# Kernel optimization log

Hardware: AMD Instinct MI355X
Metric: run time of the kernel (lower is better)

## Reference

```python
import jax, jax.numpy as jnp
import numpy as np
import itertools

BND = 64            # spatial_shape[0]; coords clamped to [0, BND] inclusive
G = BND + 1         # voxel grid side
OFFSETS = np.array(list(itertools.product([-1, 0, 1], repeat=3)), dtype=np.int32)  # [27,3], k=3, pad=1


def setup_inputs() -> dict:
    key = jax.random.key(0)
    k1, k2, k3 = jax.random.split(key, 3)
    B, H, W, C = 16, 64, 64, 256
    depth = jax.random.uniform(k1, (B, H, W), dtype=jnp.float32)
    N = B * (H * W + 1)  # +1 cls coord per batch row
    features = jax.random.normal(k2, (N, C), dtype=jnp.float32)
    # SubMConv3d weight, one [C_in, C_out] matrix per kernel offset (27 taps).
    # (Original zero-inits this weight; random values used for a meaningful baseline.)
    weight = jax.random.normal(k3, (27, C, C), dtype=jnp.float32) * 0.02
    return {"features": features, "depth": depth, "weight": weight}


def _coords(depth):
    # generate_3d_coords_from_depth + quantization from forward()
    B, H, W = depth.shape
    y, x = jnp.meshgrid(jnp.arange(H, dtype=jnp.float32) / (H - 1),
                        jnp.arange(W, dtype=jnp.float32) / (W - 1), indexing='ij')
    zmin = depth.min(axis=(1, 2), keepdims=True)
    zmax = depth.max(axis=(1, 2), keepdims=True)
    z = (depth - zmin) / (zmax - zmin + 1e-8)
    coords = jnp.stack([jnp.broadcast_to(x, (B, H, W)),
                        jnp.broadcast_to(y, (B, H, W)), z], axis=-1)  # [B,H,W,3]
    coord = coords.reshape(B, H * W, 3)
    coord = jnp.clip(jnp.round(coord * BND), 0, BND).astype(jnp.int32)
    cls = jnp.zeros((B, 1, 3), dtype=jnp.int32)  # cls token coord per batch row
    return jnp.concatenate([cls, coord], axis=1).reshape(-1, 3)  # [N,3]


def _subm_conv(features, coord, weight):
    # Submanifold sparse 3D conv: output only at active sites; gather active
    # neighbors per kernel offset, GEMM, accumulate.
    N = features.shape[0]
    lin = (coord[:, 0] * G + coord[:, 1]) * G + coord[:, 2]  # [N]
    # voxel -> point-index map; duplicates resolved deterministically via max
    idx_map = jnp.full((G * G * G,), -1, dtype=jnp.int32).at[lin].max(
        jnp.arange(N, dtype=jnp.int32))
    offs = jnp.asarray(OFFSETS)                      # [27,3]
    nb = coord[None, :, :] + offs[:, None, :]        # [27,N,3]
    inb = jnp.all((nb >= 0) & (nb <= BND), axis=-1)  # [27,N]
    nbc = jnp.clip(nb, 0, BND)
    nlin = (nbc[..., 0] * G + nbc[..., 1]) * G + nbc[..., 2]
    nid = idx_map[nlin]                              # [27,N]
    valid = inb & (nid >= 0)

    def body(acc, xs):
        nid_k, val_k, Wk = xs
        g = jnp.where(val_k[:, None], features[jnp.maximum(nid_k, 0)], 0.0)  # gather [N,C]
        return acc + g @ Wk, None

    out0 = jnp.zeros((N, weight.shape[-1]), dtype=features.dtype)
    out, _ = jax.lax.scan(body, out0, (nid, valid, weight))  # 27 gather-GEMM steps
    return out


def reference(features, depth, weight):
    coord = _coords(depth)
    return _subm_conv(features.astype(jnp.float32), coord, weight)
```

## Files before the change

### kernel.cpp

```cpp
#include <hip/hip_runtime.h>

#define NPTS 65552
#define MPAD 65664
#define NVOX 274625

typedef unsigned short u16;
typedef __attribute__((ext_vector_type(8))) short bf16x8;
typedef __attribute__((ext_vector_type(4))) float f32x4;
typedef __attribute__((ext_vector_type(4))) unsigned short us4;

__device__ __forceinline__ u16 f2bf(float f) {
  unsigned int u = __float_as_uint(f);
  return (u16)((u + 0x7FFFu + ((u >> 16) & 1u)) >> 16);
}

__global__ void coords_kernel(const float* __restrict__ depth, int* __restrict__ pcoord) {
  int b = blockIdx.x, tid = threadIdx.x;
  const float* d = depth + b * 4096;
  float mn = 1e30f, mx = -1e30f;
  for (int p = tid; p < 4096; p += 256) {
    float v = d[p];
    mn = fminf(mn, v);
    mx = fmaxf(mx, v);
  }
  __shared__ float smn[256], smx[256];
  smn[tid] = mn; smx[tid] = mx;
  __syncthreads();
  for (int s = 128; s > 0; s >>= 1) {
    if (tid < s) {
      smn[tid] = fminf(smn[tid], smn[tid + s]);
      smx[tid] = fmaxf(smx[tid], smx[tid + s]);
    }
    __syncthreads();
  }
  mn = smn[0]; mx = smx[0];
  float den = mx - mn + 1e-8f;
  for (int p = tid; p < 4096; p += 256) {
    int i = p >> 6, j = p & 63;
    float x = (float)j / 63.0f;
    float y = (float)i / 63.0f;
    float z = (d[p] - mn) / den;
    int cx = (int)rintf(x * 64.0f);
    int cy = (int)rintf(y * 64.0f);
    int cz = (int)rintf(z * 64.0f);
    cx = min(max(cx, 0), 64); cy = min(max(cy, 0), 64); cz = min(max(cz, 0), 64);
    pcoord[b * 4097 + 1 + p] = cx | (cy << 8) | (cz << 16);
  }
  if (tid == 0) pcoord[b * 4097] = 0;
}

__global__ void init_idx(int* __restrict__ m) {
  int i = blockIdx.x * 256 + threadIdx.x;
  if (i < NVOX) m[i] = -1;
}

__global__ void scatter_idx(const int* __restrict__ pcoord, int* __restrict__ m) {
  int n = blockIdx.x * 256 + threadIdx.x;
  if (n >= NPTS) return;
  int c = pcoord[n];
  int lin = ((c & 255) * 65 + ((c >> 8) & 255)) * 65 + ((c >> 16) & 255);
  atomicMax(&m[lin], n);
}

__global__ void nbr_kernel(const int* __restrict__ pcoord, const int* __restrict__ m,
                           int* __restrict__ nid) {
  int n = blockIdx.x * 256 + threadIdx.x;
  if (n >= MPAD) return;
  if (n >= NPTS) {
    for (int k = 0; k < 27; ++k) nid[k * MPAD + n] = NPTS;
    return;
  }
  int c = pcoord[n];
  int cx = c & 255, cy = (c >> 8) & 255, cz = (c >> 16) & 255;
#pragma unroll
  for (int k = 0; k < 27; ++k) {
    int nx = cx + k / 9 - 1;
    int ny = cy + (k / 3) % 3 - 1;
    int nz = cz + k % 3 - 1;
    int id = NPTS;
    if (((unsigned)nx <= 64u) && ((unsigned)ny <= 64u) && ((unsigned)nz <= 64u)) {
      int v = m[(nx * 65 + ny) * 65 + nz];
      if (v >= 0) id = v;
    }
    nid[k * MPAD + n] = id;
  }
}

__global__ void conv_feat(const float* __restrict__ f, u16* __restrict__ o) {
  int q = blockIdx.x * 256 + threadIdx.x;
  if (q >= (NPTS + 1) * 64) return;
  us4 r;
  if (q < NPTS * 64) {
    float4 v = ((const float4*)f)[q];
    r.x = f2bf(v.x); r.y = f2bf(v.y); r.z = f2bf(v.z); r.w = f2bf(v.w);
  } else {
    r.x = 0; r.y = 0; r.z = 0; r.w = 0;
  }
  ((us4*)o)[q] = r;
}

__global__ void conv_wt2(const float* __restrict__ w, u16* __restrict__ wt2) {
  int u = blockIdx.x * 256 + threadIdx.x;
  int e = u & 7, row = (u >> 3) & 255, lk = (u >> 11) & 3, ks = (u >> 13) & 7, ko = u >> 16;
  int ci = ks * 32 + lk * 8 + e;
  wt2[u] = f2bf(w[ko * 65536 + ci * 256 + row]);
}

__device__ __forceinline__ void gload16(const void* g, unsigned int lds_off) {
  __builtin_amdgcn_global_load_lds(
      (__attribute__((address_space(1))) void*)(size_t)g,
      (__attribute__((address_space(3))) void*)(unsigned int)lds_off,
      16, 0, 0);
}

__global__ __launch_bounds__(512) void gemm_kernel(const u16* __restrict__ feat,
                                                   const u16* __restrict__ wt,
                                                   const int* __restrict__ nid,
                                                   float* __restrict__ out) {
  __shared__ u16 As[3 * 4096];
  __shared__ u16 Bs[3 * 8192];
  int bm = blockIdx.x;
  int tid = threadIdx.x;
  int w = tid >> 6, l = tid & 63;
  int wr = w >> 2, wc = w & 3;
  int lm = l & 15, lk = l >> 4;

  unsigned A0 = (unsigned)(size_t)&As[0];
  unsigned B0 = (unsigned)(size_t)&Bs[0];
  const char* Asc = (const char*)&As[0];
  const char* Bsc = (const char*)&Bs[0];

  const char* featc = (const char*)feat;
  const char* wtc = (const char*)wt;

  int row_l = (w << 4) + (l >> 2);
  int gmA = bm * 128 + row_l;
  int cA16 = (((l & 3) ^ ((row_l >> 1) & 3)) << 4);
  int aswz = lk ^ ((lm >> 1) & 3);

  f32x4 acc[4][4];
#pragma unroll
  for (int m = 0; m < 4; ++m)
#pragma unroll
    for (int n = 0; n < 4; ++n) acc[m][n] = (f32x4){0.f, 0.f, 0.f, 0.f};

  int nv = nid[gmA];
  int nv_next = nv;

  {
    gload16(featc + ((size_t)nv << 9) + cA16, A0 + (w << 10));
    const char* bs0 = wtc + (w << 11) + (l << 4);
    gload16(bs0, B0 + (w << 11));
    gload16(bs0 + 1024, B0 + (w << 11) + 1024);
    gload16(featc + ((size_t)nv << 9) + 64 + cA16, A0 + 8192 + (w << 10));
    const char* bs1 = wtc + 16384 + (w << 11) + (l << 4);
    gload16(bs1, B0 + 16384 + (w << 11));
    gload16(bs1 + 1024, B0 + 16384 + (w << 11) + 1024);
  }

  unsigned a0 = 0, a1 = 8192, a2 = 16384;
  unsigned b0 = 0, b1 = 16384, b2 = 32768;

  for (int ko = 0; ko < 27; ++ko) {
#pragma unroll
    for (int ks = 0; ks < 8; ++ks) {
      if (ko == 26 && ks == 7) {
        asm volatile("s_waitcnt vmcnt(0)" ::: "memory");
      } else if (ks == 1) {
        asm volatile("s_waitcnt vmcnt(4)" ::: "memory");
      } else {
        asm volatile("s_waitcnt vmcnt(3)" ::: "memory");
      }
      __builtin_amdgcn_s_barrier();

      if (ks == 0 && ko < 26) nv_next = nid[(ko + 1) * MPAD + gmA];

      if (!(ko == 26 && ks >= 6)) {
        int snv = (ks >= 6) ? nv_next : nv;
        gload16(featc + ((size_t)snv << 9) + (((ks + 2) & 7) << 6) + cA16,
                A0 + a2 + (w << 10));
        const char* bs = wtc + ((size_t)(ko * 8 + ks + 2) << 14) + (w << 11) + (l << 4);
        gload16(bs, B0 + b2 + (w << 11));
        gload16(bs + 1024, B0 + b2 + (w << 11) + 1024);
      }

      const bf16x8* Av = (const bf16x8*)(Asc + a0);
      const bf16x8* Bv = (const bf16x8*)(Bsc + b0);
      bf16x8 a[4], b[4];
#pragma unroll
      for (int m = 0; m < 4; ++m)
        a[m] = Av[(((wr << 6) + (m << 4) + lm) << 2) + aswz];
#pragma unroll
      for (int n = 0; n < 4; ++n) b[n] = Bv[(lk << 8) + (wc << 6) + (n << 4) + lm];
      __builtin_amdgcn_s_setprio(1);
#pragma unroll
      for (int m = 0; m < 4; ++m)
#pragma unroll
        for (int n = 0; n < 4; ++n)
          acc[m][n] = __builtin_amdgcn_mfma_f32_16x16x32_bf16(a[m], b[n], acc[m][n], 0, 0, 0);
      __builtin_amdgcn_s_setprio(0);

      unsigned ta = a0; a0 = a1; a1 = a2; a2 = ta;
      unsigned tb = b0; b0 = b1; b1 = b2; b2 = tb;
    }
    nv = nv_next;
  }

#pragma unroll
  for (int m = 0; m < 4; ++m) {
#pragma unroll
    for (int i = 0; i < 4; ++i) {
      int gr2 = bm * 128 + (wr << 6) + (m << 4) + (lk << 2) + i;
      if (gr2 < NPTS) {
        float* po = out + (size_t)gr2 * 256 + (wc << 6) + lm;
#pragma unroll
        for (int n = 0; n < 4; ++n) po[n << 4] = acc[m][n][i];
      }
    }
  }
}

extern "C" void kernel_launch(void* const* d_in, const int* in_sizes, int n_in,
                              void* d_out, int out_size, void* d_ws, size_t ws_size,
                              hipStream_t stream) {
  const float* features = (const float*)d_in[0];
  const float* depth = (const float*)d_in[1];
  const float* weight = (const float*)d_in[2];
  float* out = (float*)d_out;
  char* ws = (char*)d_ws;

  int* idx_map = (int*)(ws + 0);
  int* pcoord  = (int*)(ws + 1098752);
  int* nid     = (int*)(ws + 1361152);
  u16* feat_bf = (u16*)(ws + 8452864);
  u16* wt_bf   = (u16*)(ws + 42016256);

  coords_kernel<<<16, 256, 0, stream>>>(depth, pcoord);
  init_idx<<<(NVOX + 255) / 256, 256, 0, stream>>>(idx_map);
  scatter_idx<<<(NPTS + 255) / 256, 256, 0, stream>>>(pcoord, idx_map);
  nbr_kernel<<<(MPAD + 255) / 256, 256, 0, stream>>>(pcoord, idx_map, nid);
  conv_feat<<<((NPTS + 1) * 64 + 255) / 256, 256, 0, stream>>>(features, feat_bf);
  conv_wt2<<<27 * 65536 / 256, 256, 0, stream>>>(weight, wt_bf);
  gemm_kernel<<<513, 512, 0, stream>>>(feat_bf, wt_bf, nid, out);
}
```

Before: 260.0 us.

## Switch gather-GEMM to 32x32x16 MFMA with 256-row block tiles

```diff
diff --git a/kernel.cpp b/kernel.cpp
--- a/kernel.cpp
+++ b/kernel.cpp
@@ -1,12 +1,12 @@
 #include <hip/hip_runtime.h>
 
 #define NPTS 65552
-#define MPAD 65664
+#define MPAD 65792
 #define NVOX 274625
 
 typedef unsigned short u16;
 typedef __attribute__((ext_vector_type(8))) short bf16x8;
-typedef __attribute__((ext_vector_type(4))) float f32x4;
+typedef __attribute__((ext_vector_type(16))) float f32x16;
 typedef __attribute__((ext_vector_type(4))) unsigned short us4;
 
 __device__ __forceinline__ u16 f2bf(float f) {
@@ -113,17 +113,17 @@
       16, 0, 0);
 }
 
-__global__ __launch_bounds__(512) void gemm_kernel(const u16* __restrict__ feat,
-                                                   const u16* __restrict__ wt,
-                                                   const int* __restrict__ nid,
-                                                   float* __restrict__ out) {
-  __shared__ u16 As[3 * 4096];
+__global__ __launch_bounds__(512, 2) void gemm_kernel(const u16* __restrict__ feat,
+                                                      const u16* __restrict__ wt,
+                                                      const int* __restrict__ nid,
+                                                      float* __restrict__ out) {
+  __shared__ u16 As[3 * 8192];
   __shared__ u16 Bs[3 * 8192];
   int bm = blockIdx.x;
   int tid = threadIdx.x;
   int w = tid >> 6, l = tid & 63;
   int wr = w >> 2, wc = w & 3;
-  int lm = l & 15, lk = l >> 4;
+  int l31 = l & 31, lh = l >> 5;
 
   unsigned A0 = (unsigned)(size_t)&As[0];
   unsigned B0 = (unsigned)(size_t)&Bs[0];
@@ -133,33 +133,39 @@
   const char* featc = (const char*)feat;
   const char* wtc = (const char*)wt;
 
-  int row_l = (w << 4) + (l >> 2);
-  int gmA = bm * 128 + row_l;
-  int cA16 = (((l & 3) ^ ((row_l >> 1) & 3)) << 4);
-  int aswz = lk ^ ((lm >> 1) & 3);
-
-  f32x4 acc[4][4];
+  int rA = (w << 5) + (l >> 2);
+  int gmA0 = bm * 256 + rA;
+  int gmA1 = gmA0 + 16;
+  int cA = (((l & 3) ^ ((rA >> 1) & 3)) << 4);
+  unsigned stW = (unsigned)(w << 11);
+  unsigned bSrcW = (unsigned)((w << 11) + (l << 4));
+  int aswz = (l31 >> 1) & 3;
+
+  f32x16 acc[4][2];
 #pragma unroll
   for (int m = 0; m < 4; ++m)
 #pragma unroll
-    for (int n = 0; n < 4; ++n) acc[m][n] = (f32x4){0.f, 0.f, 0.f, 0.f};
-
-  int nv = nid[gmA];
-  int nv_next = nv;
+    for (int n = 0; n < 2; ++n)
+#pragma unroll
+      for (int i = 0; i < 16; ++i) acc[m][n][i] = 0.f;
+
+  int nv0 = nid[gmA0], nv1 = nid[gmA1];
+  int nv0n = nv0, nv1n = nv1;
 
   {
-    gload16(featc + ((size_t)nv << 9) + cA16, A0 + (w << 10));
-    const char* bs0 = wtc + (w << 11) + (l << 4);
-    gload16(bs0, B0 + (w << 11));
-    gload16(bs0 + 1024, B0 + (w << 11) + 1024);
-    gload16(featc + ((size_t)nv << 9) + 64 + cA16, A0 + 8192 + (w << 10));
-    const char* bs1 = wtc + 16384 + (w << 11) + (l << 4);
-    gload16(bs1, B0 + 16384 + (w << 11));
-    gload16(bs1 + 1024, B0 + 16384 + (w << 11) + 1024);
-  }
-
-  unsigned a0 = 0, a1 = 8192, a2 = 16384;
-  unsigned b0 = 0, b1 = 16384, b2 = 32768;
+    const char* a0s = featc + ((size_t)nv0 << 9) + cA;
+    const char* a1s = featc + ((size_t)nv1 << 9) + cA;
+    gload16(a0s, A0 + stW);
+    gload16(a1s, A0 + stW + 1024);
+    gload16(wtc + bSrcW, B0 + stW);
+    gload16(wtc + bSrcW + 1024, B0 + stW + 1024);
+    gload16(a0s + 64, A0 + 16384 + stW);
+    gload16(a1s + 64, A0 + 16384 + stW + 1024);
+    gload16(wtc + 16384 + bSrcW, B0 + 16384 + stW);
+    gload16(wtc + 16384 + bSrcW + 1024, B0 + 16384 + stW + 1024);
+  }
+
+  unsigned a0 = 0, a1 = 16384, a2 = 32768;
 
   for (int ko = 0; ko < 27; ++ko) {
 #pragma unroll
@@ -167,54 +173,66 @@
       if (ko == 26 && ks == 7) {
         asm volatile("s_waitcnt vmcnt(0)" ::: "memory");
       } else if (ks == 1) {
+        asm volatile("s_waitcnt vmcnt(6)" ::: "memory");
+      } else {
         asm volatile("s_waitcnt vmcnt(4)" ::: "memory");
-      } else {
-        asm volatile("s_waitcnt vmcnt(3)" ::: "memory");
       }
       __builtin_amdgcn_s_barrier();
 
-      if (ks == 0 && ko < 26) nv_next = nid[(ko + 1) * MPAD + gmA];
+      if (ks == 0 && ko < 26) {
+        nv0n = nid[(ko + 1) * MPAD + gmA0];
+        nv1n = nid[(ko + 1) * MPAD + gmA1];
+      }
 
       if (!(ko == 26 && ks >= 6)) {
-        int snv = (ks >= 6) ? nv_next : nv;
-        gload16(featc + ((size_t)snv << 9) + (((ks + 2) & 7) << 6) + cA16,
-                A0 + a2 + (w << 10));
-        const char* bs = wtc + ((size_t)(ko * 8 + ks + 2) << 14) + (w << 11) + (l << 4);
-        gload16(bs, B0 + b2 + (w << 11));
-        gload16(bs + 1024, B0 + b2 + (w << 11) + 1024);
+        int s0 = (ks >= 6) ? nv0n : nv0;
+        int s1 = (ks >= 6) ? nv1n : nv1;
+        int kb = ((ks + 2) & 7) << 6;
+        gload16(featc + ((size_t)s0 << 9) + kb + cA, A0 + a2 + stW);
+        gload16(featc + ((size_t)s1 << 9) + kb + cA, A0 + a2 + stW + 1024);
+        const char* bs = wtc + ((size_t)(ko * 8 + ks + 2) << 14) + bSrcW;
+        gload16(bs, B0 + a2 + stW);
+        gload16(bs + 1024, B0 + a2 + stW + 1024);
       }
 
       const bf16x8* Av = (const bf16x8*)(Asc + a0);
-      const bf16x8* Bv = (const bf16x8*)(Bsc + b0);
-      bf16x8 a[4], b[4];
+      const bf16x8* Bv = (const bf16x8*)(Bsc + a0);
+      bf16x8 a[4][2], b[2][2];
 #pragma unroll
       for (int m = 0; m < 4; ++m)
-        a[m] = Av[(((wr << 6) + (m << 4) + lm) << 2) + aswz];
-#pragma unroll
-      for (int n = 0; n < 4; ++n) b[n] = Bv[(lk << 8) + (wc << 6) + (n << 4) + lm];
+#pragma unroll
+        for (int kk = 0; kk < 2; ++kk)
+          a[m][kk] = Av[((wr << 7) + (m << 5) + l31) * 4 + (((kk << 1) + lh) ^ aswz)];
+#pragma unroll
+      for (int n = 0; n < 2; ++n)
+#pragma unroll
+        for (int kk = 0; kk < 2; ++kk)
+          b[n][kk] = Bv[(((kk << 1) + lh) << 8) + (wc << 6) + (n << 5) + l31];
       __builtin_amdgcn_s_setprio(1);
 #pragma unroll
       for (int m = 0; m < 4; ++m)
 #pragma unroll
-        for (int n = 0; n < 4; ++n)
-          acc[m][n] = __builtin_amdgcn_mfma_f32_16x16x32_bf16(a[m], b[n], acc[m][n], 0, 0, 0);
+        for (int n = 0; n < 2; ++n)
+#pragma unroll
+          for (int kk = 0; kk < 2; ++kk)
+            acc[m][n] = __builtin_amdgcn_mfma_f32_32x32x16_bf16(a[m][kk], b[n][kk],
+                                                                acc[m][n], 0, 0, 0);
       __builtin_amdgcn_s_setprio(0);
 
       unsigned ta = a0; a0 = a1; a1 = a2; a2 = ta;
-      unsigned tb = b0; b0 = b1; b1 = b2; b2 = tb;
-    }
-    nv = nv_next;
+    }
+    nv0 = nv0n; nv1 = nv1n;
   }
 
 #pragma unroll
   for (int m = 0; m < 4; ++m) {
 #pragma unroll
-    for (int i = 0; i < 4; ++i) {
-      int gr2 = bm * 128 + (wr << 6) + (m << 4) + (lk << 2) + i;
+    for (int i = 0; i < 16; ++i) {
+      int gr2 = bm * 256 + (wr << 7) + (m << 5) + (i & 3) + ((i >> 2) << 3) + (lh << 2);
       if (gr2 < NPTS) {
-        float* po = out + (size_t)gr2 * 256 + (wc << 6) + lm;
-#pragma unroll
-        for (int n = 0; n < 4; ++n) po[n << 4] = acc[m][n][i];
+        float* po = out + (size_t)gr2 * 256 + (wc << 6) + l31;
+#pragma unroll
+        for (int n = 0; n < 2; ++n) po[n << 5] = acc[m][n][i];
       }
     }
   }
@@ -232,8 +250,8 @@
   int* idx_map = (int*)(ws + 0);
   int* pcoord  = (int*)(ws + 1098752);
   int* nid     = (int*)(ws + 1361152);
-  u16* feat_bf = (u16*)(ws + 8452864);
-  u16* wt_bf   = (u16*)(ws + 42016256);
+  u16* feat_bf = (u16*)(ws + 8466688);
+  u16* wt_bf   = (u16*)(ws + 42029824);
 
   coords_kernel<<<16, 256, 0, stream>>>(depth, pcoord);
   init_idx<<<(NVOX + 255) / 256, 256, 0, stream>>>(idx_map);
@@ -241,5 +259,5 @@
   nbr_kernel<<<(MPAD + 255) / 256, 256, 0, stream>>>(pcoord, idx_map, nid);
   conv_feat<<<((NPTS + 1) * 64 + 255) / 256, 256, 0, stream>>>(features, feat_bf);
   conv_wt2<<<27 * 65536 / 256, 256, 0, stream>>>(weight, wt_bf);
-  gemm_kernel<<<513, 512, 0, stream>>>(feat_bf, wt_bf, nid, out);
-}
+  gemm_kernel<<<257, 512, 0, stream>>>(feat_bf, wt_bf, nid, out);
+}
```

Result: slower. 362.0 us (+39.2%).

## Use 4-wave blocks with each wave computing a 128x64 output tile

Applied to the files above, without the earlier changes.

```diff
diff --git a/kernel.cpp b/kernel.cpp
--- a/kernel.cpp
+++ b/kernel.cpp
@@ -113,16 +113,15 @@
       16, 0, 0);
 }
 
-__global__ __launch_bounds__(512) void gemm_kernel(const u16* __restrict__ feat,
-                                                   const u16* __restrict__ wt,
-                                                   const int* __restrict__ nid,
-                                                   float* __restrict__ out) {
+__global__ __launch_bounds__(256, 2) void gemm_kernel(const u16* __restrict__ feat,
+                                                      const u16* __restrict__ wt,
+                                                      const int* __restrict__ nid,
+                                                      float* __restrict__ out) {
   __shared__ u16 As[3 * 4096];
   __shared__ u16 Bs[3 * 8192];
   int bm = blockIdx.x;
   int tid = threadIdx.x;
   int w = tid >> 6, l = tid & 63;
-  int wr = w >> 2, wc = w & 3;
   int lm = l & 15, lk = l >> 4;
 
   unsigned A0 = (unsigned)(size_t)&As[0];
@@ -133,29 +132,35 @@
   const char* featc = (const char*)feat;
   const char* wtc = (const char*)wt;
 
-  int row_l = (w << 4) + (l >> 2);
-  int gmA = bm * 128 + row_l;
-  int cA16 = (((l & 3) ^ ((row_l >> 1) & 3)) << 4);
+  int rA = (w << 5) + (l >> 2);
+  int gmA0 = bm * 128 + rA;
+  int gmA1 = gmA0 + 16;
+  int cA = (((l & 3) ^ ((rA >> 1) & 3)) << 4);
+  size_t bSrc = (size_t)((w << 12) + (l << 4));
   int aswz = lk ^ ((lm >> 1) & 3);
 
-  f32x4 acc[4][4];
-#pragma unroll
-  for (int m = 0; m < 4; ++m)
+  f32x4 acc[8][4];
+#pragma unroll
+  for (int m = 0; m < 8; ++m)
 #pragma unroll
     for (int n = 0; n < 4; ++n) acc[m][n] = (f32x4){0.f, 0.f, 0.f, 0.f};
 
-  int nv = nid[gmA];
-  int nv_next = nv;
+  int nv0 = nid[gmA0], nv1 = nid[gmA1];
+  int nv0n = nv0, nv1n = nv1;
 
   {
-    gload16(featc + ((size_t)nv << 9) + cA16, A0 + (w << 10));
-    const char* bs0 = wtc + (w << 11) + (l << 4);
-    gload16(bs0, B0 + (w << 11));
-    gload16(bs0 + 1024, B0 + (w << 11) + 1024);
-    gload16(featc + ((size_t)nv << 9) + 64 + cA16, A0 + 8192 + (w << 10));
-    const char* bs1 = wtc + 16384 + (w << 11) + (l << 4);
-    gload16(bs1, B0 + 16384 + (w << 11));
-    gload16(bs1 + 1024, B0 + 16384 + (w << 11) + 1024);
+    const char* a0s = featc + ((size_t)nv0 << 9) + cA;
+    const char* a1s = featc + ((size_t)nv1 << 9) + cA;
+    gload16(a0s, A0 + (w << 11));
+    gload16(a1s, A0 + (w << 11) + 1024);
+    const char* bs0 = wtc + bSrc;
+#pragma unroll
+    for (int c = 0; c < 4; ++c) gload16(bs0 + (c << 10), B0 + (w << 12) + (c << 10));
+    gload16(a0s + 64, A0 + 8192 + (w << 11));
+    gload16(a1s + 64, A0 + 8192 + (w << 11) + 1024);
+    const char* bs1 = wtc + 16384 + bSrc;
+#pragma unroll
+    for (int c = 0; c < 4; ++c) gload16(bs1 + (c << 10), B0 + 16384 + (w << 12) + (c << 10));
   }
 
   unsigned a0 = 0, a1 = 8192, a2 = 16384;
@@ -166,53 +171,66 @@
     for (int ks = 0; ks < 8; ++ks) {
       if (ko == 26 && ks == 7) {
         asm volatile("s_waitcnt vmcnt(0)" ::: "memory");
-      } else if (ks == 1) {
-        asm volatile("s_waitcnt vmcnt(4)" ::: "memory");
+      } else if (ks == 1 && ko < 26) {
+        asm volatile("s_waitcnt vmcnt(8)" ::: "memory");
       } else {
-        asm volatile("s_waitcnt vmcnt(3)" ::: "memory");
+        asm volatile("s_waitcnt vmcnt(6)" ::: "memory");
       }
       __builtin_amdgcn_s_barrier();
 
-      if (ks == 0 && ko < 26) nv_next = nid[(ko + 1) * MPAD + gmA];
+      if (ks == 0 && ko < 26) {
+        nv0n = nid[(ko + 1) * MPAD + gmA0];
+        nv1n = nid[(ko + 1) * MPAD + gmA1];
+      }
 
       if (!(ko == 26 && ks >= 6)) {
-        int snv = (ks >= 6) ? nv_next : nv;
-        gload16(featc + ((size_t)snv << 9) + (((ks + 2) & 7) << 6) + cA16,
-                A0 + a2 + (w << 10));
-        const char* bs = wtc + ((size_t)(ko * 8 + ks + 2) << 14) + (w << 11) + (l << 4);
-        gload16(bs, B0 + b2 + (w << 11));
-        gload16(bs + 1024, B0 + b2 + (w << 11) + 1024);
+        int s0 = (ks >= 6) ? nv0n : nv0;
+        int s1 = (ks >= 6) ? nv1n : nv1;
+        int kb = ((ks + 2) & 7) << 6;
+        const char* a0s = featc + ((size_t)s0 << 9) + kb + cA;
+        const char* a1s = featc + ((size_t)s1 << 9) + kb + cA;
+        gload16(a0s, A0 + a2 + (w << 11));
+        gload16(a1s, A0 + a2 + (w << 11) + 1024);
+        const char* bs = wtc + ((size_t)(ko * 8 + ks + 2) << 14) + bSrc;
+#pragma unroll
+        for (int c = 0; c < 4; ++c)
+          gload16(bs + (c << 10), B0 + b2 + (w << 12) + (c << 10));
       }
 
       const bf16x8* Av = (const bf16x8*)(Asc + a0);
       const bf16x8* Bv = (const bf16x8*)(Bsc + b0);
-      bf16x8 a[4], b[4];
-#pragma unroll
-      for (int m = 0; m < 4; ++m)
-        a[m] = Av[(((wr << 6) + (m << 4) + lm) << 2) + aswz];
-#pragma unroll
-      for (int n = 0; n < 4; ++n) b[n] = Bv[(lk << 8) + (wc << 6) + (n << 4) + lm];
-      __builtin_amdgcn_s_setprio(1);
-#pragma unroll
-      for (int m = 0; m < 4; ++m)
-#pragma unroll
-        for (int n = 0; n < 4; ++n)
-          acc[m][n] = __builtin_amdgcn_mfma_f32_16x16x32_bf16(a[m], b[n], acc[m][n], 0, 0, 0);
-      __builtin_amdgcn_s_setprio(0);
-
-      unsigned ta = a0; a0 = a1; a1 = a2; a2 = ta;
-      unsigned tb = b0; b0 = b1; b1 = b2; b2 = tb;
-    }
-    nv = nv_next;
-  }
-
-#pragma unroll
-  for (int m = 0; m < 4; ++m) {
+      bf16x8 bfr[4];
+#pragma unroll
+      for (int n = 0; n < 4; ++n) bfr[n] = Bv[(lk << 8) + (w << 6) + (n << 4) + lm];
+#pragma unroll
+      for (int h = 0; h < 2; ++h) {
+        bf16x8 afr[4];
+#pragma unroll
+        for (int m4 = 0; m4 < 4; ++m4)
+          afr[m4] = Av[(((h << 6) + (m4 << 4) + lm) << 2) + aswz];
+        __builtin_amdgcn_s_setprio(1);
+#pragma unroll
+        for (int m4 = 0; m4 < 4; ++m4)
+#pragma unroll
+          for (int n = 0; n < 4; ++n)
+            acc[h * 4 + m4][n] = __builtin_amdgcn_mfma_f32_16x16x32_bf16(
+                afr[m4], bfr[n], acc[h * 4 + m4][n], 0, 0, 0);
+        __builtin_amdgcn_s_setprio(0);
+      }
+
+      { unsigned t_ = a0; a0 = a1; a1 = a2; a2 = t_; }
+      { unsigned t_ = b0; b0 = b1; b1 = b2; b2 = t_; }
+    }
+    nv0 = nv0n; nv1 = nv1n;
+  }
+
+#pragma unroll
+  for (int m = 0; m < 8; ++m) {
 #pragma unroll
     for (int i = 0; i < 4; ++i) {
-      int gr2 = bm * 128 + (wr << 6) + (m << 4) + (lk << 2) + i;
+      int gr2 = bm * 128 + (m << 4) + (lk << 2) + i;
       if (gr2 < NPTS) {
-        float* po = out + (size_t)gr2 * 256 + (wc << 6) + lm;
+        float* po = out + (size_t)gr2 * 256 + (w << 6) + lm;
 #pragma unroll
         for (int n = 0; n < 4; ++n) po[n << 4] = acc[m][n][i];
       }
@@ -241,5 +259,5 @@
   nbr_kernel<<<(MPAD + 255) / 256, 256, 0, stream>>>(pcoord, idx_map, nid);
   conv_feat<<<((NPTS + 1) * 64 + 255) / 256, 256, 0, stream>>>(features, feat_bf);
   conv_wt2<<<27 * 65536 / 256, 256, 0, stream>>>(weight, wt_bf);
-  gemm_kernel<<<513, 512, 0, stream>>>(feat_bf, wt_bf, nid, out);
-}
+  gemm_kernel<<<513, 256, 0, stream>>>(feat_bf, wt_bf, nid, out);
+}
```

Measured after the change: 286.4 us. 10.1% more time.

## Load weight fragments directly into registers instead of staging through LDS

Applied to the files above, without the earlier changes.

```diff
diff --git a/kernel.cpp b/kernel.cpp
--- a/kernel.cpp
+++ b/kernel.cpp
@@ -113,12 +113,11 @@
       16, 0, 0);
 }
 
-__global__ __launch_bounds__(512) void gemm_kernel(const u16* __restrict__ feat,
-                                                   const u16* __restrict__ wt,
-                                                   const int* __restrict__ nid,
-                                                   float* __restrict__ out) {
+__global__ __launch_bounds__(512, 4) void gemm_kernel(const u16* __restrict__ feat,
+                                                      const u16* __restrict__ wt,
+                                                      const int* __restrict__ nid,
+                                                      float* __restrict__ out) {
   __shared__ u16 As[3 * 4096];
-  __shared__ u16 Bs[3 * 8192];
   int bm = blockIdx.x;
   int tid = threadIdx.x;
   int w = tid >> 6, l = tid & 63;
@@ -126,9 +125,7 @@
   int lm = l & 15, lk = l >> 4;
 
   unsigned A0 = (unsigned)(size_t)&As[0];
-  unsigned B0 = (unsigned)(size_t)&Bs[0];
   const char* Asc = (const char*)&As[0];
-  const char* Bsc = (const char*)&Bs[0];
 
   const char* featc = (const char*)feat;
   const char* wtc = (const char*)wt;
@@ -136,6 +133,7 @@
   int row_l = (w << 4) + (l >> 2);
   int gmA = bm * 128 + row_l;
   int cA16 = (((l & 3) ^ ((row_l >> 1) & 3)) << 4);
+  size_t bOff = (size_t)(((lk << 8) + (wc << 6) + lm) << 4);
   int aswz = lk ^ ((lm >> 1) & 3);
 
   f32x4 acc[4][4];
@@ -143,65 +141,66 @@
   for (int m = 0; m < 4; ++m)
 #pragma unroll
     for (int n = 0; n < 4; ++n) acc[m][n] = (f32x4){0.f, 0.f, 0.f, 0.f};
+
+  bf16x8 bcur[4], bnxt[4];
 
   int nv = nid[gmA];
   int nv_next = nv;
 
   {
+#pragma unroll
+    for (int n = 0; n < 4; ++n)
+      bcur[n] = *(const bf16x8*)(wtc + bOff + ((size_t)n << 8));
     gload16(featc + ((size_t)nv << 9) + cA16, A0 + (w << 10));
-    const char* bs0 = wtc + (w << 11) + (l << 4);
-    gload16(bs0, B0 + (w << 11));
-    gload16(bs0 + 1024, B0 + (w << 11) + 1024);
     gload16(featc + ((size_t)nv << 9) + 64 + cA16, A0 + 8192 + (w << 10));
-    const char* bs1 = wtc + 16384 + (w << 11) + (l << 4);
-    gload16(bs1, B0 + 16384 + (w << 11));
-    gload16(bs1 + 1024, B0 + 16384 + (w << 11) + 1024);
   }
 
   unsigned a0 = 0, a1 = 8192, a2 = 16384;
-  unsigned b0 = 0, b1 = 16384, b2 = 32768;
 
   for (int ko = 0; ko < 27; ++ko) {
 #pragma unroll
     for (int ks = 0; ks < 8; ++ks) {
-      if (ko == 26 && ks == 7) {
+      if (ko == 0 && ks == 0) {
+        asm volatile("s_waitcnt vmcnt(1)" ::: "memory");
+      } else if (ko == 26 && ks == 7) {
         asm volatile("s_waitcnt vmcnt(0)" ::: "memory");
-      } else if (ks == 1) {
-        asm volatile("s_waitcnt vmcnt(4)" ::: "memory");
       } else {
-        asm volatile("s_waitcnt vmcnt(3)" ::: "memory");
+        asm volatile("s_waitcnt vmcnt(5)" ::: "memory");
       }
       __builtin_amdgcn_s_barrier();
 
       if (ks == 0 && ko < 26) nv_next = nid[(ko + 1) * MPAD + gmA];
+
+      if (!(ko == 26 && ks == 7)) {
+        const char* bp = wtc + ((size_t)(ko * 8 + ks + 1) << 14) + bOff;
+#pragma unroll
+        for (int n = 0; n < 4; ++n)
+          bnxt[n] = *(const bf16x8*)(bp + ((size_t)n << 8));
+      }
 
       if (!(ko == 26 && ks >= 6)) {
         int snv = (ks >= 6) ? nv_next : nv;
-        gload16(featc + ((size_t)snv << 9) + (((ks + 2) & 7) << 6) + cA16,
+        gload16(featc + ((size_t)snv << 9) + ((((ks) + 2) & 7) << 6) + cA16,
                 A0 + a2 + (w << 10));
-        const char* bs = wtc + ((size_t)(ko * 8 + ks + 2) << 14) + (w << 11) + (l << 4);
-        gload16(bs, B0 + b2 + (w << 11));
-        gload16(bs + 1024, B0 + b2 + (w << 11) + 1024);
       }
 
       const bf16x8* Av = (const bf16x8*)(Asc + a0);
-      const bf16x8* Bv = (const bf16x8*)(Bsc + b0);
-      bf16x8 a[4], b[4];
+      bf16x8 afr[4];
 #pragma unroll
       for (int m = 0; m < 4; ++m)
-        a[m] = Av[(((wr << 6) + (m << 4) + lm) << 2) + aswz];
-#pragma unroll
-      for (int n = 0; n < 4; ++n) b[n] = Bv[(lk << 8) + (wc << 6) + (n << 4) + lm];
+        afr[m] = Av[(((wr << 6) + (m << 4) + lm) << 2) + aswz];
       __builtin_amdgcn_s_setprio(1);
 #pragma unroll
       for (int m = 0; m < 4; ++m)
 #pragma unroll
         for (int n = 0; n < 4; ++n)
-          acc[m][n] = __builtin_amdgcn_mfma_f32_16x16x32_bf16(a[m], b[n], acc[m][n], 0, 0, 0);
+          acc[m][n] = __builtin_amdgcn_mfma_f32_16x16x32_bf16(afr[m], bcur[n],
+                                                              acc[m][n], 0, 0, 0);
       __builtin_amdgcn_s_setprio(0);
 
-      unsigned ta = a0; a0 = a1; a1 = a2; a2 = ta;
-      unsigned tb = b0; b0 = b1; b1 = b2; b2 = tb;
+#pragma unroll
+      for (int n = 0; n < 4; ++n) bcur[n] = bnxt[n];
+      { unsigned t_ = a0; a0 = a1; a1 = a2; a2 = t_; }
     }
     nv = nv_next;
   }
```

After: 334.0 us. +28.5%, slower.
